# Kernel optimization log

Hardware: AMD Instinct MI355X
Metric: run time of the kernel (lower is better)

## Reference

```python
import jax, jax.numpy as jnp
import numpy as np

DIM, H, KV, HD = 2048, 32, 8, 64
NREP = H // KV
EPS = 1e-6
NEG = -1e30


def _rope(x, cos, sin):
    # x: [B,S,h,HD], cos/sin: [S,HD//2]
    xr, xi = x[..., 0::2], x[..., 1::2]
    c = cos[None, :, None, :]
    s = sin[None, :, None, :]
    out = jnp.stack([xr * c - xi * s, xr * s + xi * c], axis=-1)
    return out.reshape(x.shape)


def _rmsnorm(x, w):
    xf = x.astype(jnp.float32)
    inv = jax.lax.rsqrt(jnp.mean(xf * xf, axis=-1, keepdims=True) + EPS)
    return (xf * inv * w).astype(x.dtype)


def setup_inputs() -> dict:
    key = jax.random.key(0)
    ks = jax.random.split(key, 9)
    B, S = 1, 2048
    x = jax.random.normal(ks[0], (B, S, DIM), jnp.float32)
    cos = jax.random.uniform(ks[1], (S, HD // 2), jnp.float32)
    sin = jax.random.uniform(ks[2], (S, HD // 2), jnp.float32)
    sc = 1.0 / np.sqrt(DIM)
    wq = jax.random.normal(ks[3], (DIM, DIM), jnp.float32) * sc
    wk = jax.random.normal(ks[4], (KV * HD, DIM), jnp.float32) * sc
    wv = jax.random.normal(ks[5], (KV * HD, DIM), jnp.float32) * sc
    wo = jax.random.normal(ks[6], (DIM, DIM), jnp.float32) * sc
    wg = jax.random.normal(ks[7], (DIM, DIM), jnp.float32) * sc
    qn = jnp.ones((HD,), jnp.float32)
    kn = jnp.ones((HD,), jnp.float32)
    return {"x": x, "cos": cos, "sin": sin, "wq": wq, "wk": wk, "wv": wv,
            "wo": wo, "wg": wg, "qn": qn, "kn": kn}


def reference(x, cos, sin, wq, wk, wv, wo, wg, qn, kn):
    B, S, _ = x.shape
    q = (x @ wq.T).reshape(B, S, H, HD)
    k = (x @ wk.T).reshape(B, S, KV, HD)
    v = (x @ wv.T).reshape(B, S, KV, HD)
    q = _rope(q, cos, sin)
    k = _rope(k, cos, sin)
    q = _rmsnorm(q, qn)
    k = _rmsnorm(k, kn)
    # GQA without materializing repeat_kv: head h = g*NREP + r uses kv head g
    qg = q.reshape(B, S, KV, NREP, HD)
    scale = 1.0 / np.sqrt(HD)
    scores = jnp.einsum('bqgrd,bkgd->bgrqk', qg, k) * scale  # [B,KV,NREP,S,S]
    causal = jnp.tril(jnp.ones((S, S), bool))
    scores = jnp.where(causal, scores, NEG)
    attn = jax.nn.softmax(scores, axis=-1)
    o = jnp.einsum('bgrqk,bkgd->bqgrd', attn, v).reshape(B, S, DIM)
    o = o * jax.nn.sigmoid(x @ wg.T)
    return o @ wo.T
```

## Files before the change

### kernel.cpp

```cpp
#include <hip/hip_runtime.h>
#include <stdint.h>

typedef unsigned short u16;
typedef unsigned int u32;
typedef __bf16 bf16x8 __attribute__((ext_vector_type(8)));
typedef __bf16 bf16x2 __attribute__((ext_vector_type(2)));
typedef float f32x4 __attribute__((ext_vector_type(4)));

__device__ __forceinline__ float bf2f(u16 u) {
  union { unsigned int i; float f; } v; v.i = ((unsigned int)u) << 16; return v.f;
}
__device__ __forceinline__ u16 f2bf(float f) {
  union { float f; unsigned int i; } v; v.f = f;
  unsigned int r = v.i + 0x7fffu + ((v.i >> 16) & 1u);
  return (u16)(r >> 16);
}
__device__ __forceinline__ void ld16(const void* g, void* l) {
  __builtin_amdgcn_global_load_lds(
      (const __attribute__((address_space(1))) unsigned int*)g,
      (__attribute__((address_space(3))) unsigned int*)l, 16, 0, 0);
}

__global__ __launch_bounds__(256) void k_cast(
    const float* __restrict__ s0, u16* __restrict__ d0,
    const float* __restrict__ s1, u16* __restrict__ d1,
    const float* __restrict__ s2, u16* __restrict__ d2,
    const float* __restrict__ s3, u16* __restrict__ d3,
    const float* __restrict__ s4, u16* __restrict__ d4,
    const float* __restrict__ s5, u16* __restrict__ d5)
{
  int b = blockIdx.x;
  const float* s; u16* d;
  if (b < 4096)       { s = s0; d = d0; }
  else if (b < 8192)  { s = s1; d = d1; b -= 4096; }
  else if (b < 9216)  { s = s2; d = d2; b -= 8192; }
  else if (b < 10240) { s = s3; d = d3; b -= 9216; }
  else if (b < 14336) { s = s4; d = d4; b -= 10240; }
  else                { s = s5; d = d5; b -= 14336; }
  const int i = (b * 256 + threadIdx.x) * 4;
  const float4 v = *(const float4*)(s + i);
  ushort4 o;
  o.x = f2bf(v.x); o.y = f2bf(v.y); o.z = f2bf(v.z); o.w = f2bf(v.w);
  *(ushort4*)(d + i) = o;
}

template <typename OT>
__device__ __forceinline__ void gemm_body(
    const u16* __restrict__ A, int lda,
    const u16* __restrict__ B, int ldb,
    OT* __restrict__ C, int ldc, int K,
    u16* As, u16* Bs)
{
  const int tid = threadIdx.x;
  const int wave = tid >> 6, lane = tid & 63;
  const int wrow = (wave >> 1) * 64, wcol = (wave & 1) * 64;
  const int fr = lane & 15, kg = lane >> 4;
  const int srl = lane >> 3;
  const int scg = (lane & 7) ^ srl;

  f32x4 acc[4][4];
  const f32x4 z = {0.f, 0.f, 0.f, 0.f};
  for (int i = 0; i < 4; i++) for (int j = 0; j < 4; j++) acc[i][j] = z;

  const u16* Ag = A + (size_t)(wave * 8 + srl) * lda + scg * 8;
  const u16* Bg = B + (size_t)(wave * 8 + srl) * ldb + scg * 8;
  u16* Asw = As + wave * 8 * 64;
  u16* Bsw = Bs + wave * 8 * 64;
  const int sxr = fr & 7;

  for (int k0 = 0; k0 < K; k0 += 64) {
    for (int i = 0; i < 4; i++) {
      ld16(Ag + k0 + (size_t)(i * 32) * lda, Asw + i * 32 * 64);
      ld16(Bg + k0 + (size_t)(i * 32) * ldb, Bsw + i * 32 * 64);
    }
    __syncthreads();
    bf16x8 af[4][2], bfr[4][2];
    for (int i = 0; i < 4; i++)
      for (int h = 0; h < 2; h++) {
        af[i][h]  = *(const bf16x8*)&As[(wrow + i * 16 + fr) * 64 + (((h * 4 + kg) ^ sxr)) * 8];
        bfr[i][h] = *(const bf16x8*)&Bs[(wcol + i * 16 + fr) * 64 + (((h * 4 + kg) ^ sxr)) * 8];
      }
    for (int h = 0; h < 2; h++)
      for (int mi = 0; mi < 4; mi++)
        for (int ni = 0; ni < 4; ni++)
          acc[mi][ni] = __builtin_amdgcn_mfma_f32_16x16x32_bf16(af[mi][h], bfr[ni][h], acc[mi][ni], 0, 0, 0);
    __syncthreads();
  }
  const int er = kg * 4, ec = fr;
  for (int mi = 0; mi < 4; mi++)
    for (int ni = 0; ni < 4; ni++)
      for (int r = 0; r < 4; r++) {
        const float v = acc[mi][ni][r];
        OT* p = C + (size_t)(wrow + mi * 16 + er + r) * ldc + wcol + ni * 16 + ec;
        if constexpr (sizeof(OT) == 2) *p = (OT)f2bf(v); else *p = (OT)v;
      }
}

__global__ __launch_bounds__(256) void k_gemm_qkvg(
    const u16* __restrict__ x, const u16* __restrict__ wq, const u16* __restrict__ wk,
    const u16* __restrict__ wv, const u16* __restrict__ wg, u16* __restrict__ out)
{
  __shared__ __align__(16) u16 As[128 * 64];
  __shared__ __align__(16) u16 Bs[128 * 64];
  const int m0 = blockIdx.x * 128;
  const int c0 = blockIdx.y * 128;
  const u16* B; int br;
  if (c0 < 2048)      { B = wq; br = c0; }
  else if (c0 < 2560) { B = wk; br = c0 - 2048; }
  else if (c0 < 3072) { B = wv; br = c0 - 2560; }
  else                { B = wg; br = c0 - 3072; }
  gemm_body<u16>(x + (size_t)m0 * 2048, 2048, B + (size_t)br * 2048, 2048,
                 out + (size_t)m0 * 5120 + c0, 5120, 2048, As, Bs);
}

__global__ __launch_bounds__(256) void k_gemm_out(
    const u16* __restrict__ a, const u16* __restrict__ wo, float* __restrict__ out)
{
  __shared__ __align__(16) u16 As[128 * 64];
  __shared__ __align__(16) u16 Bs[128 * 64];
  const int m0 = blockIdx.x * 128;
  const int c0 = blockIdx.y * 128;
  gemm_body<float>(a + (size_t)m0 * 2048, 2048, wo + (size_t)c0 * 2048, 2048,
                   out + (size_t)m0 * 2048 + c0, 2048, 2048, As, Bs);
}

__global__ __launch_bounds__(256) void k_prep(
    u16* __restrict__ qkvg, const float* __restrict__ cosp, const float* __restrict__ sinp,
    const float* __restrict__ qn, const float* __restrict__ kn, u16* __restrict__ vt)
{
  __shared__ u16 Ls[64 * 72];
  if (blockIdx.x < 10240) {
    const int wid = (blockIdx.x * 256 + threadIdx.x) >> 6;
    const int lane = threadIdx.x & 63;
    const int s = wid / 20, hp = wid - s * 20;
    const int h = hp * 2 + (lane >> 5);
    const int j = lane & 31;
    u16* base; const float* wn;
    if (h < 32) { base = qkvg + (size_t)s * 5120 + h * 64;                wn = qn; }
    else        { base = qkvg + (size_t)s * 5120 + 2048 + (h - 32) * 64; wn = kn; }
    const unsigned int u = *(const unsigned int*)(base + 2 * j);
    const float xr = bf2f((u16)(u & 0xffffu)), xi = bf2f((u16)(u >> 16));
    const float c = cosp[s * 32 + j], sn = sinp[s * 32 + j];
    const float o0 = xr * c - xi * sn;
    const float o1 = xr * sn + xi * c;
    float ss = o0 * o0 + o1 * o1;
    for (int m = 1; m <= 16; m <<= 1) ss += __shfl_xor(ss, m, 64);
    const float inv = rsqrtf(ss * (1.0f / 64.0f) + 1e-6f);
    const u16 r0 = f2bf(o0 * inv * wn[2 * j]);
    const u16 r1 = f2bf(o1 * inv * wn[2 * j + 1]);
    *(unsigned int*)(base + 2 * j) = (unsigned int)r0 | ((unsigned int)r1 << 16);
  } else {
    const int bb = blockIdx.x - 10240;
    const int s0 = (bb & 31) * 64, g0 = (bb >> 5) * 64;
    const int tid = threadIdx.x;
    const int lr = tid >> 4, lc = (tid & 15) * 4;
    for (int p = 0; p < 4; p++) {
      const int r = p * 16 + lr;
      *(ushort4*)&Ls[r * 72 + lc] = *(const ushort4*)&qkvg[(size_t)(s0 + r) * 5120 + 2560 + g0 + lc];
    }
    __syncthreads();
    for (int p = 0; p < 4; p++) {
      const int r = p * 16 + lr;
      ushort4 o;
      o.x = Ls[(lc + 0) * 72 + r];
      o.y = Ls[(lc + 1) * 72 + r];
      o.z = Ls[(lc + 2) * 72 + r];
      o.w = Ls[(lc + 3) * 72 + r];
      *(ushort4*)&vt[(size_t)(g0 + r) * 2048 + s0 + lc] = o;
    }
  }
}

__global__ __launch_bounds__(256, 3) void k_attn_part(
    const u16* __restrict__ qkvg, const u16* __restrict__ vt,
    u16* __restrict__ part, float* __restrict__ ml)
{
  __shared__ __align__(16) u16 SMEM[3 * 64 * 128];
  u16* Ks = SMEM;
  u16* Vs = SMEM + 8192;
  u16* Ps = SMEM + 16384;
  const int c = blockIdx.x, gp = blockIdx.y;
  const int g = gp >> 1, h0 = (gp >> 1) * 4 + (gp & 1) * 2;
  int qt, ci;
  if (c < 8)       { qt = c;                 ci = 0; }
  else if (c < 24) { qt = 8 + ((c - 8) >> 1);  ci = (c - 8) & 1; }
  else if (c < 48) { qt = 16 + (c - 24) / 3;   ci = (c - 24) % 3; }
  else             { qt = 24 + ((c - 48) >> 2); ci = (c - 48) & 3; }
  const int kb0 = ci * 512;
  const int kend = min(kb0 + 512, (qt + 1) * 64);
  const int q0 = qt * 64;
  const int tid = threadIdx.x, wave = tid >> 6, lane = tid & 63;
  const int fr = lane & 15, kg = lane >> 4;
  const int sx = fr & 7;

  {
    const u16* Qg = qkvg + (size_t)(q0 + wave * 16 + (lane >> 4)) * 5120 + h0 * 64 + (lane & 15) * 8;
#pragma unroll
    for (int i = 0; i < 4; i++)
      ld16(Qg + (size_t)(i * 4) * 5120, SMEM + (wave * 16 + i * 4) * 128);
  }
  __syncthreads();
  bf16x8 aq[2][2];
#pragma unroll
  for (int hh = 0; hh < 2; hh++)
#pragma unroll
    for (int hf = 0; hf < 2; hf++)
      aq[hh][hf] = *(const bf16x8*)&SMEM[(wave * 16 + fr) * 128 + hh * 64 + hf * 32 + kg * 8];
  __syncthreads();

  f32x4 o[2][4];
  const f32x4 z = {0.f, 0.f, 0.f, 0.f};
#pragma unroll
  for (int hh = 0; hh < 2; hh++)
#pragma unroll
    for (int i = 0; i < 4; i++) o[hh][i] = z;
  float L[2] = {0.f, 0.f};
  const int qrow = q0 + wave * 16 + fr;
  const int prow = wave * 16 + fr;

  const int krl = wave * 8 + (lane >> 3);
  const int kcg = (lane & 7) ^ (krl & 7);
  const int vrl = wave * 4 + kg;
  const int vcg = fr ^ (vrl & 7);

  for (int kb = kb0; kb < kend; kb += 128) {
    {
      const u16* Kg = qkvg + (size_t)(kb + krl) * 5120 + 2048 + g * 64 + kcg * 8;
#pragma unroll
      for (int i = 0; i < 4; i++)
        ld16(Kg + (size_t)(i * 32) * 5120, Ks + (i * 32 + wave * 8) * 64);
    }
    {
      const u16* Vg = vt + (size_t)(g * 64 + vrl) * 2048 + kb + vcg * 8;
#pragma unroll
      for (int i = 0; i < 4; i++)
        ld16(Vg + (size_t)(i * 16) * 2048, Vs + (i * 16 + wave * 4) * 128);
    }
    __syncthreads();

    const bool masked = (kb + 127 > q0 + wave * 16);
    u32* Ps32 = (u32*)Ps;
    const int pb32 = prow * 64;

#pragma unroll
    for (int hh = 0; hh < 2; hh++) {
      f32x4 sc[8];
#pragma unroll
      for (int i = 0; i < 8; i++) sc[i] = z;
      __builtin_amdgcn_s_setprio(1);
#pragma unroll
      for (int ni = 0; ni < 8; ni++) {
        const bf16x8 bk0 = *(const bf16x8*)&Ks[(ni * 16 + fr) * 64 + ((kg ^ sx)) * 8];
        const bf16x8 bk1 = *(const bf16x8*)&Ks[(ni * 16 + fr) * 64 + (((kg + 4) ^ sx)) * 8];
        sc[ni] = __builtin_amdgcn_mfma_f32_16x16x32_bf16(bk0, aq[hh][0], sc[ni], 0, 0, 0);
        sc[ni] = __builtin_amdgcn_mfma_f32_16x16x32_bf16(bk1, aq[hh][1], sc[ni], 0, 0, 0);
      }
      __builtin_amdgcn_s_setprio(0);

      float Lh = 0.f;
      if (masked) {
#pragma unroll
        for (int ni = 0; ni < 8; ni++) {
          const int dlim = qrow - (kb + ni * 16 + kg * 4);
          float p0 = exp2f(fmaf(sc[ni][0], 0.18033688f, -11.5415603f));
          float p1 = exp2f(fmaf(sc[ni][1], 0.18033688f, -11.5415603f));
          float p2 = exp2f(fmaf(sc[ni][2], 0.18033688f, -11.5415603f));
          float p3 = exp2f(fmaf(sc[ni][3], 0.18033688f, -11.5415603f));
          p0 = (0 <= dlim) ? p0 : 0.f;
          p1 = (1 <= dlim) ? p1 : 0.f;
          p2 = (2 <= dlim) ? p2 : 0.f;
          p3 = (3 <= dlim) ? p3 : 0.f;
          Lh += (p0 + p1) + (p2 + p3);
          bf16x2 w0, w1;
          w0[0] = (__bf16)p0; w0[1] = (__bf16)p1;
          w1[0] = (__bf16)p2; w1[1] = (__bf16)p3;
          const int a = pb32 + ((2 * ni + (kg >> 1)) ^ sx) * 4 + (kg & 1) * 2;
          *(bf16x2*)&Ps32[a]     = w0;
          *(bf16x2*)&Ps32[a + 1] = w1;
        }
      } else {
#pragma unroll
        for (int ni = 0; ni < 8; ni++) {
          float p0 = exp2f(fmaf(sc[ni][0], 0.18033688f, -11.5415603f));
          float p1 = exp2f(fmaf(sc[ni][1], 0.18033688f, -11.5415603f));
          float p2 = exp2f(fmaf(sc[ni][2], 0.18033688f, -11.5415603f));
          float p3 = exp2f(fmaf(sc[ni][3], 0.18033688f, -11.5415603f));
          Lh += (p0 + p1) + (p2 + p3);
          bf16x2 w0, w1;
          w0[0] = (__bf16)p0; w0[1] = (__bf16)p1;
          w1[0] = (__bf16)p2; w1[1] = (__bf16)p3;
          const int a = pb32 + ((2 * ni + (kg >> 1)) ^ sx) * 4 + (kg & 1) * 2;
          *(bf16x2*)&Ps32[a]     = w0;
          *(bf16x2*)&Ps32[a + 1] = w1;
        }
      }
      L[hh] += Lh;

      __builtin_amdgcn_s_setprio(1);
#pragma unroll
      for (int k0 = 0; k0 < 128; k0 += 32) {
        const bf16x8 ap = *(const bf16x8*)&Ps[prow * 128 + ((((k0 >> 3) + kg)) ^ sx) * 8];
#pragma unroll
        for (int ni = 0; ni < 4; ni++) {
          const bf16x8 bv = *(const bf16x8*)&Vs[(ni * 16 + fr) * 128 + (((k0 >> 3) + kg) ^ sx) * 8];
          o[hh][ni] = __builtin_amdgcn_mfma_f32_16x16x32_bf16(ap, bv, o[hh][ni], 0, 0, 0);
        }
      }
      __builtin_amdgcn_s_setprio(0);
    }
    __syncthreads();
  }

#pragma unroll
  for (int hh = 0; hh < 2; hh++) {
    float Lh = L[hh];
    Lh += __shfl_xor(Lh, 16, 64);
    Lh += __shfl_xor(Lh, 32, 64);
    const int h = h0 + hh;
    const int pbase = (h * 80 + c) * 4096;
#pragma unroll
    for (int ni = 0; ni < 4; ni++)
#pragma unroll
      for (int r = 0; r < 4; r++)
        part[pbase + (wave * 16 + kg * 4 + r) * 64 + ni * 16 + fr] = f2bf(o[hh][ni][r]);
    if (lane < 16) ml[(h * 80 + c) * 64 + wave * 16 + fr] = Lh;
  }
}

__global__ __launch_bounds__(256) void k_attn_comb(
    const u16* __restrict__ part, const float* __restrict__ ml,
    const u16* __restrict__ qkvg, u16* __restrict__ aout)
{
  const int qt = blockIdx.x, h = blockIdx.y;
  const int w = threadIdx.x >> 6, lane = threadIdx.x & 63;
  int cb, nch;
  if (qt < 8)       { cb = qt;               nch = 1; }
  else if (qt < 16) { cb = 8 + 2 * (qt - 8);  nch = 2; }
  else if (qt < 24) { cb = 24 + 3 * (qt - 16); nch = 3; }
  else              { cb = 48 + 4 * (qt - 24); nch = 4; }
  for (int r = 0; r < 16; r++) {
    const int rl = w * 16 + r;
    const int row = qt * 64 + rl;
    float L = 0.f, o = 0.f;
    for (int cc = 0; cc < nch; cc++) {
      L += ml[(h * 80 + cb + cc) * 64 + rl];
      o += bf2f(part[(h * 80 + cb + cc) * 4096 + rl * 64 + lane]);
    }
    const float gv = bf2f(qkvg[(size_t)row * 5120 + 3072 + h * 64 + lane]);
    const float sig = 1.0f / (1.0f + __expf(-gv));
    aout[(size_t)row * 2048 + h * 64 + lane] = f2bf(o / L * sig);
  }
}

extern "C" void kernel_launch(void* const* d_in, const int* in_sizes, int n_in,
                              void* d_out, int out_size, void* d_ws, size_t ws_size,
                              hipStream_t stream)
{
  const float* x  = (const float*)d_in[0];
  const float* cs = (const float*)d_in[1];
  const float* sn = (const float*)d_in[2];
  const float* wq = (const float*)d_in[3];
  const float* wk = (const float*)d_in[4];
  const float* wv = (const float*)d_in[5];
  const float* wo = (const float*)d_in[6];
  const float* wg = (const float*)d_in[7];
  const float* qn = (const float*)d_in[8];
  const float* kn = (const float*)d_in[9];
  float* out = (float*)d_out;

  u16* xb   = (u16*)d_ws;
  u16* wqb  = xb  + (size_t)4194304;
  u16* wkb  = wqb + (size_t)4194304;
  u16* wvb  = wkb + (size_t)1048576;
  u16* wgb  = wvb + (size_t)1048576;
  u16* wob  = wgb + (size_t)4194304;
  u16* qkvg = wob + (size_t)4194304;
  u16* vt   = qkvg + (size_t)2048 * 5120;
  u16* aws  = vt   + (size_t)512 * 2048;

  u16*   part = xb;
  float* ml   = (float*)(xb + (size_t)32 * 80 * 4096);

  k_cast<<<dim3(18432), 256, 0, stream>>>(x, xb, wq, wqb, wk, wkb, wv, wvb, wo, wob, wg, wgb);
  k_gemm_qkvg<<<dim3(16, 40), 256, 0, stream>>>(xb, wqb, wkb, wvb, wgb, qkvg);
  k_prep<<<dim3(10240 + 256), 256, 0, stream>>>(qkvg, cs, sn, qn, kn, vt);
  k_attn_part<<<dim3(80, 16), 256, 0, stream>>>(qkvg, vt, part, ml);
  k_attn_comb<<<dim3(32, 32), 256, 0, stream>>>(part, ml, qkvg, aws);
  k_gemm_out<<<dim3(16, 16), 256, 0, stream>>>(aws, wob, out);
}
```

Measured before the change: 292.2 us.

## Double-buffer K/V tiles in attention partial kernel to overlap loads with MFMA

Splits the K/V shared-memory staging into two buffers and prefetches the next 128-key tile while the current one is computed, waiting with a partial vmcnt before each barrier. This aims to hide global-to-LDS load latency behind the QK and PV matrix multiplies. LDS use rises from 48KB to 80KB and launch bounds drop from 3 to 2 blocks per CU, which reduces occupancy. On the last iteration the prefetch reloads the current tile redundantly, and replacing __syncthreads with raw s_barrier relies on the manual waitcnt for correctness.

```diff
diff --git a/kernel.cpp b/kernel.cpp
--- a/kernel.cpp
+++ b/kernel.cpp
@@ -171,14 +171,12 @@
   }
 }
 
-__global__ __launch_bounds__(256, 3) void k_attn_part(
+__global__ __launch_bounds__(256, 2) void k_attn_part(
     const u16* __restrict__ qkvg, const u16* __restrict__ vt,
     u16* __restrict__ part, float* __restrict__ ml)
 {
-  __shared__ __align__(16) u16 SMEM[3 * 64 * 128];
-  u16* Ks = SMEM;
-  u16* Vs = SMEM + 8192;
-  u16* Ps = SMEM + 16384;
+  __shared__ __align__(16) u16 SMEM[5 * 8192];
+  u16* Ps = SMEM + 32768;
   const int c = blockIdx.x, gp = blockIdx.y;
   const int g = gp >> 1, h0 = (gp >> 1) * 4 + (gp & 1) * 2;
   int qt, ci;
@@ -223,20 +221,28 @@
   const int vrl = wave * 4 + kg;
   const int vcg = fr ^ (vrl & 7);
 
+  auto stageKV = [&](int kb_, u16* Kd) {
+    const u16* Kg = qkvg + (size_t)(kb_ + krl) * 5120 + 2048 + g * 64 + kcg * 8;
+#pragma unroll
+    for (int i = 0; i < 4; i++)
+      ld16(Kg + (size_t)(i * 32) * 5120, Kd + (i * 32 + wave * 8) * 64);
+    u16* Vd = Kd + 8192;
+    const u16* Vg = vt + (size_t)(g * 64 + vrl) * 2048 + kb_ + vcg * 8;
+#pragma unroll
+    for (int i = 0; i < 4; i++)
+      ld16(Vg + (size_t)(i * 16) * 2048, Vd + (i * 16 + wave * 4) * 128);
+  };
+
+  stageKV(kb0, SMEM);
+  int bufsel = 0;
+
   for (int kb = kb0; kb < kend; kb += 128) {
-    {
-      const u16* Kg = qkvg + (size_t)(kb + krl) * 5120 + 2048 + g * 64 + kcg * 8;
-#pragma unroll
-      for (int i = 0; i < 4; i++)
-        ld16(Kg + (size_t)(i * 32) * 5120, Ks + (i * 32 + wave * 8) * 64);
-    }
-    {
-      const u16* Vg = vt + (size_t)(g * 64 + vrl) * 2048 + kb + vcg * 8;
-#pragma unroll
-      for (int i = 0; i < 4; i++)
-        ld16(Vg + (size_t)(i * 16) * 2048, Vs + (i * 16 + wave * 4) * 128);
-    }
-    __syncthreads();
+    u16* Kc = SMEM + bufsel * 16384;
+    u16* Vc = Kc + 8192;
+    const int kbn = (kb + 128 < kend) ? kb + 128 : kb;
+    stageKV(kbn, SMEM + (bufsel ^ 1) * 16384);
+    asm volatile("s_waitcnt vmcnt(8)" ::: "memory");
+    __builtin_amdgcn_s_barrier();
 
     const bool masked = (kb + 127 > q0 + wave * 16);
     u32* Ps32 = (u32*)Ps;
@@ -250,8 +256,8 @@
       __builtin_amdgcn_s_setprio(1);
 #pragma unroll
       for (int ni = 0; ni < 8; ni++) {
-        const bf16x8 bk0 = *(const bf16x8*)&Ks[(ni * 16 + fr) * 64 + ((kg ^ sx)) * 8];
-        const bf16x8 bk1 = *(const bf16x8*)&Ks[(ni * 16 + fr) * 64 + (((kg + 4) ^ sx)) * 8];
+        const bf16x8 bk0 = *(const bf16x8*)&Kc[(ni * 16 + fr) * 64 + ((kg ^ sx)) * 8];
+        const bf16x8 bk1 = *(const bf16x8*)&Kc[(ni * 16 + fr) * 64 + (((kg + 4) ^ sx)) * 8];
         sc[ni] = __builtin_amdgcn_mfma_f32_16x16x32_bf16(bk0, aq[hh][0], sc[ni], 0, 0, 0);
         sc[ni] = __builtin_amdgcn_mfma_f32_16x16x32_bf16(bk1, aq[hh][1], sc[ni], 0, 0, 0);
       }
@@ -302,13 +308,14 @@
         const bf16x8 ap = *(const bf16x8*)&Ps[prow * 128 + ((((k0 >> 3) + kg)) ^ sx) * 8];
 #pragma unroll
         for (int ni = 0; ni < 4; ni++) {
-          const bf16x8 bv = *(const bf16x8*)&Vs[(ni * 16 + fr) * 128 + (((k0 >> 3) + kg) ^ sx) * 8];
+          const bf16x8 bv = *(const bf16x8*)&Vc[(ni * 16 + fr) * 128 + (((k0 >> 3) + kg) ^ sx) * 8];
           o[hh][ni] = __builtin_amdgcn_mfma_f32_16x16x32_bf16(ap, bv, o[hh][ni], 0, 0, 0);
         }
       }
       __builtin_amdgcn_s_setprio(0);
     }
-    __syncthreads();
+    __builtin_amdgcn_s_barrier();
+    bufsel ^= 1;
   }
 
 #pragma unroll
```

Result: no change. 297.3 us (+1.7%).

## Batch QK^T for both heads, use raw v_exp_f32, and widen P stores

Applied to the files above, without the earlier changes.

Computes the score MFMAs for both heads of the wave up front, sharing each K fragment load, instead of alternating score, softmax and PV per head. This gives the scheduler more independent MFMA work to overlap with the exp and softmax ALU work. exp2f is replaced by inline-asm v_exp_f32, which drops the range-handling code, and the two bf16x2 LDS stores become one bf16x4 store. The cost is about 32 more live accumulator registers for the second score set, which can lower occupancy, plus slightly different exp precision.

```diff
diff --git a/kernel.cpp b/kernel.cpp
--- a/kernel.cpp
+++ b/kernel.cpp
@@ -4,6 +4,7 @@
 typedef unsigned short u16;
 typedef unsigned int u32;
 typedef __bf16 bf16x8 __attribute__((ext_vector_type(8)));
+typedef __bf16 bf16x4 __attribute__((ext_vector_type(4)));
 typedef __bf16 bf16x2 __attribute__((ext_vector_type(2)));
 typedef float f32x4 __attribute__((ext_vector_type(4)));
 
@@ -14,6 +15,9 @@
   union { float f; unsigned int i; } v; v.f = f;
   unsigned int r = v.i + 0x7fffu + ((v.i >> 16) & 1u);
   return (u16)(r >> 16);
+}
+__device__ __forceinline__ float fastexp2(float x) {
+  float r; asm("v_exp_f32 %0, %1" : "=v"(r) : "v"(x)); return r;
 }
 __device__ __forceinline__ void ld16(const void* g, void* l) {
   __builtin_amdgcn_global_load_lds(
@@ -242,72 +246,112 @@
     u32* Ps32 = (u32*)Ps;
     const int pb32 = prow * 64;
 
-#pragma unroll
-    for (int hh = 0; hh < 2; hh++) {
-      f32x4 sc[8];
-#pragma unroll
-      for (int i = 0; i < 8; i++) sc[i] = z;
-      __builtin_amdgcn_s_setprio(1);
-#pragma unroll
-      for (int ni = 0; ni < 8; ni++) {
-        const bf16x8 bk0 = *(const bf16x8*)&Ks[(ni * 16 + fr) * 64 + ((kg ^ sx)) * 8];
-        const bf16x8 bk1 = *(const bf16x8*)&Ks[(ni * 16 + fr) * 64 + (((kg + 4) ^ sx)) * 8];
-        sc[ni] = __builtin_amdgcn_mfma_f32_16x16x32_bf16(bk0, aq[hh][0], sc[ni], 0, 0, 0);
-        sc[ni] = __builtin_amdgcn_mfma_f32_16x16x32_bf16(bk1, aq[hh][1], sc[ni], 0, 0, 0);
-      }
-      __builtin_amdgcn_s_setprio(0);
-
+    f32x4 s0[8], s1[8];
+#pragma unroll
+    for (int i = 0; i < 8; i++) { s0[i] = z; s1[i] = z; }
+    __builtin_amdgcn_s_setprio(1);
+#pragma unroll
+    for (int ni = 0; ni < 8; ni++) {
+      const bf16x8 bk0 = *(const bf16x8*)&Ks[(ni * 16 + fr) * 64 + ((kg ^ sx)) * 8];
+      const bf16x8 bk1 = *(const bf16x8*)&Ks[(ni * 16 + fr) * 64 + (((kg + 4) ^ sx)) * 8];
+      s0[ni] = __builtin_amdgcn_mfma_f32_16x16x32_bf16(bk0, aq[0][0], s0[ni], 0, 0, 0);
+      s0[ni] = __builtin_amdgcn_mfma_f32_16x16x32_bf16(bk1, aq[0][1], s0[ni], 0, 0, 0);
+      s1[ni] = __builtin_amdgcn_mfma_f32_16x16x32_bf16(bk0, aq[1][0], s1[ni], 0, 0, 0);
+      s1[ni] = __builtin_amdgcn_mfma_f32_16x16x32_bf16(bk1, aq[1][1], s1[ni], 0, 0, 0);
+    }
+    __builtin_amdgcn_s_setprio(0);
+
+    {
       float Lh = 0.f;
       if (masked) {
 #pragma unroll
         for (int ni = 0; ni < 8; ni++) {
           const int dlim = qrow - (kb + ni * 16 + kg * 4);
-          float p0 = exp2f(fmaf(sc[ni][0], 0.18033688f, -11.5415603f));
-          float p1 = exp2f(fmaf(sc[ni][1], 0.18033688f, -11.5415603f));
-          float p2 = exp2f(fmaf(sc[ni][2], 0.18033688f, -11.5415603f));
-          float p3 = exp2f(fmaf(sc[ni][3], 0.18033688f, -11.5415603f));
+          float p0 = fastexp2(fmaf(s0[ni][0], 0.18033688f, -11.5415603f));
+          float p1 = fastexp2(fmaf(s0[ni][1], 0.18033688f, -11.5415603f));
+          float p2 = fastexp2(fmaf(s0[ni][2], 0.18033688f, -11.5415603f));
+          float p3 = fastexp2(fmaf(s0[ni][3], 0.18033688f, -11.5415603f));
           p0 = (0 <= dlim) ? p0 : 0.f;
           p1 = (1 <= dlim) ? p1 : 0.f;
           p2 = (2 <= dlim) ? p2 : 0.f;
           p3 = (3 <= dlim) ? p3 : 0.f;
           Lh += (p0 + p1) + (p2 + p3);
-          bf16x2 w0, w1;
-          w0[0] = (__bf16)p0; w0[1] = (__bf16)p1;
-          w1[0] = (__bf16)p2; w1[1] = (__bf16)p3;
-          const int a = pb32 + ((2 * ni + (kg >> 1)) ^ sx) * 4 + (kg & 1) * 2;
-          *(bf16x2*)&Ps32[a]     = w0;
-          *(bf16x2*)&Ps32[a + 1] = w1;
+          bf16x4 w;
+          w[0] = (__bf16)p0; w[1] = (__bf16)p1; w[2] = (__bf16)p2; w[3] = (__bf16)p3;
+          *(bf16x4*)&Ps32[pb32 + ((2 * ni + (kg >> 1)) ^ sx) * 4 + (kg & 1) * 2] = w;
         }
       } else {
 #pragma unroll
         for (int ni = 0; ni < 8; ni++) {
-          float p0 = exp2f(fmaf(sc[ni][0], 0.18033688f, -11.5415603f));
-          float p1 = exp2f(fmaf(sc[ni][1], 0.18033688f, -11.5415603f));
-          float p2 = exp2f(fmaf(sc[ni][2], 0.18033688f, -11.5415603f));
-          float p3 = exp2f(fmaf(sc[ni][3], 0.18033688f, -11.5415603f));
+          float p0 = fastexp2(fmaf(s0[ni][0], 0.18033688f, -11.5415603f));
+          float p1 = fastexp2(fmaf(s0[ni][1], 0.18033688f, -11.5415603f));
+          float p2 = fastexp2(fmaf(s0[ni][2], 0.18033688f, -11.5415603f));
+          float p3 = fastexp2(fmaf(s0[ni][3], 0.18033688f, -11.5415603f));
           Lh += (p0 + p1) + (p2 + p3);
-          bf16x2 w0, w1;
-          w0[0] = (__bf16)p0; w0[1] = (__bf16)p1;
-          w1[0] = (__bf16)p2; w1[1] = (__bf16)p3;
-          const int a = pb32 + ((2 * ni + (kg >> 1)) ^ sx) * 4 + (kg & 1) * 2;
-          *(bf16x2*)&Ps32[a]     = w0;
-          *(bf16x2*)&Ps32[a + 1] = w1;
+          bf16x4 w;
+          w[0] = (__bf16)p0; w[1] = (__bf16)p1; w[2] = (__bf16)p2; w[3] = (__bf16)p3;
+          *(bf16x4*)&Ps32[pb32 + ((2 * ni + (kg >> 1)) ^ sx) * 4 + (kg & 1) * 2] = w;
         }
       }
-      L[hh] += Lh;
-
-      __builtin_amdgcn_s_setprio(1);
-#pragma unroll
-      for (int k0 = 0; k0 < 128; k0 += 32) {
-        const bf16x8 ap = *(const bf16x8*)&Ps[prow * 128 + ((((k0 >> 3) + kg)) ^ sx) * 8];
-#pragma unroll
-        for (int ni = 0; ni < 4; ni++) {
-          const bf16x8 bv = *(const bf16x8*)&Vs[(ni * 16 + fr) * 128 + (((k0 >> 3) + kg) ^ sx) * 8];
-          o[hh][ni] = __builtin_amdgcn_mfma_f32_16x16x32_bf16(ap, bv, o[hh][ni], 0, 0, 0);
+      L[0] += Lh;
+    }
+    __builtin_amdgcn_s_setprio(1);
+#pragma unroll
+    for (int k0 = 0; k0 < 128; k0 += 32) {
+      const bf16x8 ap = *(const bf16x8*)&Ps[prow * 128 + ((((k0 >> 3) + kg)) ^ sx) * 8];
+#pragma unroll
+      for (int ni = 0; ni < 4; ni++) {
+        const bf16x8 bv = *(const bf16x8*)&Vs[(ni * 16 + fr) * 128 + (((k0 >> 3) + kg) ^ sx) * 8];
+        o[0][ni] = __builtin_amdgcn_mfma_f32_16x16x32_bf16(ap, bv, o[0][ni], 0, 0, 0);
+      }
+    }
+    __builtin_amdgcn_s_setprio(0);
+
+    {
+      float Lh = 0.f;
+      if (masked) {
+#pragma unroll
+        for (int ni = 0; ni < 8; ni++) {
+          const int dlim = qrow - (kb + ni * 16 + kg * 4);
+          float p0 = fastexp2(fmaf(s1[ni][0], 0.18033688f, -11.5415603f));
+          float p1 = fastexp2(fmaf(s1[ni][1], 0.18033688f, -11.5415603f));
+          float p2 = fastexp2(fmaf(s1[ni][2], 0.18033688f, -11.5415603f));
+          float p3 = fastexp2(fmaf(s1[ni][3], 0.18033688f, -11.5415603f));
+          p0 = (0 <= dlim) ? p0 : 0.f;
+          p1 = (1 <= dlim) ? p1 : 0.f;
+          p2 = (2 <= dlim) ? p2 : 0.f;
+          p3 = (3 <= dlim) ? p3 : 0.f;
+          Lh += (p0 + p1) + (p2 + p3);
+          bf16x4 w;
+          w[0] = (__bf16)p0; w[1] = (__bf16)p1; w[2] = (__bf16)p2; w[3] = (__bf16)p3;
+          *(bf16x4*)&Ps32[pb32 + ((2 * ni + (kg >> 1)) ^ sx) * 4 + (kg & 1) * 2] = w;
         }
-      }
-      __builtin_amdgcn_s_setprio(0);
-    }
+      } else {
+#pragma unroll
+        for (int ni = 0; ni < 8; ni++) {
+          float p0 = fastexp2(fmaf(s1[ni][0], 0.18033688f, -11.5415603f));
+          float p1 = fastexp2(fmaf(s1[ni][1], 0.18033688f, -11.5415603f));
+          float p2 = fastexp2(fmaf(s1[ni][2], 0.18033688f, -11.5415603f));
+          float p3 = fastexp2(fmaf(s1[ni][3], 0.18033688f, -11.5415603f));
+          Lh += (p0 + p1) + (p2 + p3);
+          bf16x4 w;
+          w[0] = (__bf16)p0; w[1] = (__bf16)p1; w[2] = (__bf16)p2; w[3] = (__bf16)p3;
+          *(bf16x4*)&Ps32[pb32 + ((2 * ni + (kg >> 1)) ^ sx) * 4 + (kg & 1) * 2] = w;
+        }
+      }
+      L[1] += Lh;
+    }
+    __builtin_amdgcn_s_setprio(1);
+#pragma unroll
+    for (int k0 = 0; k0 < 128; k0 += 32) {
+      const bf16x8 ap = *(const bf16x8*)&Ps[prow * 128 + ((((k0 >> 3) + kg)) ^ sx) * 8];
+#pragma unroll
+      for (int ni = 0; ni < 4; ni++) {
+        const bf16x8 bv = *(const bf16x8*)&Vs[(ni * 16 + fr) * 128 + (((k0 >> 3) + kg) ^ sx) * 8];
+        o[1][ni] = __builtin_amdgcn_mfma_f32_16x16x32_bf16(ap, bv, o[1][ni], 0, 0, 0);
+      }
+    }
+    __builtin_amdgcn_s_setprio(0);
     __syncthreads();
   }
 
```

Measured after the change: 287.2 us. No clear change (-1.7%).
